# Kernel optimization log

Hardware: AMD Instinct MI355X
Metric: run time of the kernel (lower is better)

Reference implementation:

```python
import jax, jax.numpy as jnp
import numpy as np

E = 7       # number of experts (len(expert_details))
K = 2       # top-k routing
CAP = 3072  # per-expert capacity ~ ceil(T*K/E * 1.25)
D = 1024    # d_model
H = 4096    # d_ff = 4*d_model
T = 8192    # tokens (B=2, S=4096)


def setup_inputs() -> dict:
    key = jax.random.key(0)
    k1, k2, k3, k4 = jax.random.split(key, 4)
    x = jax.random.normal(k1, (T, D), jnp.float32)
    Wg = jax.random.normal(k2, (D, E), jnp.float32) * 0.02
    W1 = jax.random.normal(k3, (E, D, H), jnp.float32) * 0.02
    W2 = jax.random.normal(k4, (E, H, D), jnp.float32) * 0.02
    return {"x": x, "Wg": Wg, "W1": W1, "W2": W2}


def reference(x, Wg, W1, W2):
    Tn, Dn = x.shape
    # --- router ---
    gates = jax.nn.softmax(x @ Wg, axis=-1)          # [T, E]
    topw, topi = jax.lax.top_k(gates, K)             # [T, K]
    topw = topw / jnp.sum(topw, axis=-1, keepdims=True)
    flat_e = topi.reshape(-1)                        # [T*K] expert ids (int)
    flat_w = topw.reshape(-1)                        # [T*K] combine weights
    # --- position within each expert (priority = token order) ---
    onehot = jax.nn.one_hot(flat_e, E, dtype=jnp.int32)           # [T*K, E]
    pos = jnp.sum(jnp.cumsum(onehot, axis=0) * onehot, axis=-1) - 1  # [T*K]
    keep = pos < CAP
    slot = jnp.where(keep, pos, CAP)  # overflow tokens go to pad slot CAP
    # --- dispatch: scatter tokens into [E, CAP, D] buffer ---
    x_rep = jnp.repeat(x, K, axis=0)                               # [T*K, D]
    buf = jnp.zeros((E, CAP + 1, Dn), x.dtype).at[flat_e, slot].set(x_rep)[:, :CAP]
    # --- grouped expert FFN (grouped GEMMs) ---
    h = jax.nn.gelu(jnp.einsum('ecd,edh->ech', buf, W1))
    y = jnp.einsum('ech,ehd->ecd', h, W2)                          # [E, CAP, D]
    # --- combine: gather back and weight ---
    y_pad = jnp.concatenate([y, jnp.zeros((E, 1, Dn), y.dtype)], axis=1)
    out_slots = y_pad[flat_e, slot] * (flat_w * keep.astype(flat_w.dtype))[:, None]
    return out_slots.reshape(Tn, K, Dn).sum(axis=1)                # [T, D]
```

## Files before the change

### kernel.cpp

```cpp
#include <hip/hip_runtime.h>
#include <stdint.h>


#define NEXP 7
#define KTOP 2
#define CAP 3072
#define DM 1024
#define HF 4096
#define TT 8192
#define RBLK 32

typedef __bf16 bf16x8 __attribute__((ext_vector_type(8)));
typedef float f32x4 __attribute__((ext_vector_type(4)));

__device__ __forceinline__ unsigned short f2bf(float v) {
  union { float f; unsigned u; } a; a.f = v;
  unsigned r = a.u + 0x7FFFu + ((a.u >> 16) & 1u);
  return (unsigned short)(r >> 16);
}
__device__ __forceinline__ float bf2f(unsigned short h) {
  union { unsigned u; float f; } a; a.u = ((unsigned)h) << 16; return a.f;
}
__device__ __forceinline__ float gelu_t(float v) {
  float u = 0.7978845608028654f * (v + 0.044715f * v * v * v);
  float ex = __expf(2.0f * u);
  float th = 1.0f - 2.0f / (ex + 1.0f);
  return 0.5f * v * (1.0f + th);
}
__device__ __forceinline__ void gl2lds16(const void* g, void* l) {
  __builtin_amdgcn_global_load_lds(
      (const __attribute__((address_space(1))) unsigned int*)g,
      (__attribute__((address_space(3))) unsigned int*)l, 16, 0, 0);
}

__global__ void init_counts(int* counts) {
  if (threadIdx.x < NEXP) counts[threadIdx.x] = 0;
}

__global__ __launch_bounds__(256) void router_fused(
    const float* __restrict__ x, const float* __restrict__ Wg,
    int* __restrict__ counts, int* __restrict__ flatSlot,
    int* __restrict__ tokOfSlot, float* __restrict__ wOfSlot,
    unsigned short* __restrict__ xb) {
  __shared__ float sWgT[NEXP][DM];
  __shared__ int hist[NEXP], base[NEXP];
  __shared__ int pickE[RBLK * 2];
  __shared__ int pickR[RBLK * 2];
  __shared__ float pickW[RBLK * 2];
  int tid = threadIdx.x, lane = tid & 63, wave = tid >> 6;

  for (int i = tid; i < NEXP * DM; i += 256) {
    int e = i / DM, d = i - e * DM;
    sWgT[e][d] = Wg[d * NEXP + e];
  }
  if (tid < NEXP) hist[tid] = 0;
  __syncthreads();

  for (int tt = wave; tt < RBLK; tt += 4) {
    int t = blockIdx.x * RBLK + tt;
    const float4* xr = (const float4*)(x + (long)t * DM);
    double acc[NEXP];
#pragma unroll
    for (int e = 0; e < NEXP; ++e) acc[e] = 0.0;
#pragma unroll
    for (int j = 0; j < 4; ++j) {
      float4 xv = xr[j * 64 + lane];
      int d4 = (j * 64 + lane) * 4;
#pragma unroll
      for (int e = 0; e < NEXP; ++e) {
        float4 wv = *(const float4*)&sWgT[e][d4];
        acc[e] += (double)xv.x * (double)wv.x + (double)xv.y * (double)wv.y
                + (double)xv.z * (double)wv.z + (double)xv.w * (double)wv.w;
      }
    }
#pragma unroll
    for (int e = 0; e < NEXP; ++e) {
#pragma unroll
      for (int off = 32; off > 0; off >>= 1) acc[e] += __shfl_down(acc[e], off);
    }
    if (lane == 0) {
      int i1 = 0; double l1 = acc[0];
      for (int e2 = 1; e2 < NEXP; ++e2) if (acc[e2] > l1) { l1 = acc[e2]; i1 = e2; }
      int i2 = -1; double l2 = -1e300;
      for (int e2 = 0; e2 < NEXP; ++e2) if (e2 != i1 && acc[e2] > l2) { l2 = acc[e2]; i2 = e2; }
      float w1 = (float)(1.0 / (1.0 + exp(l2 - l1)));
      int r0 = atomicAdd(&hist[i1], 1);
      int r1 = atomicAdd(&hist[i2], 1);
      pickE[2 * tt] = i1;     pickR[2 * tt] = r0;     pickW[2 * tt] = w1;
      pickE[2 * tt + 1] = i2; pickR[2 * tt + 1] = r1; pickW[2 * tt + 1] = 1.0f - w1;
    }
  }
  __syncthreads();
  if (tid < NEXP) base[tid] = atomicAdd(&counts[tid], hist[tid]);
  __syncthreads();

  for (int tt = wave; tt < RBLK; tt += 4) {
    int t = blockIdx.x * RBLK + tt;
    const float4* xr = (const float4*)(x + (long)t * DM);
    float4 v0 = xr[0 * 64 + lane], v1 = xr[1 * 64 + lane];
    float4 v2 = xr[2 * 64 + lane], v3 = xr[3 * 64 + lane];
    ushort4 o0, o1, o2, o3;
    o0.x = f2bf(v0.x); o0.y = f2bf(v0.y); o0.z = f2bf(v0.z); o0.w = f2bf(v0.w);
    o1.x = f2bf(v1.x); o1.y = f2bf(v1.y); o1.z = f2bf(v1.z); o1.w = f2bf(v1.w);
    o2.x = f2bf(v2.x); o2.y = f2bf(v2.y); o2.z = f2bf(v2.z); o2.w = f2bf(v2.w);
    o3.x = f2bf(v3.x); o3.y = f2bf(v3.y); o3.z = f2bf(v3.z); o3.w = f2bf(v3.w);
#pragma unroll
    for (int p = 0; p < 2; ++p) {
      int e = pickE[2 * tt + p];
      int s = base[e] + pickR[2 * tt + p];
      int fi = t * 2 + p;
      if (lane == 0) {
        flatSlot[fi] = (s < CAP) ? s : CAP;
        if (s < CAP) { tokOfSlot[e * CAP + s] = fi; wOfSlot[e * CAP + s] = pickW[2 * tt + p]; }
      }
      if (s < CAP) {
        ushort4* dst = (ushort4*)(xb + ((long)e * CAP + s) * DM);
        dst[0 * 64 + lane] = o0; dst[1 * 64 + lane] = o1;
        dst[2 * 64 + lane] = o2; dst[3 * 64 + lane] = o3;
      }
    }
  }
}

__global__ void transcvt(const float* __restrict__ in, unsigned short* __restrict__ out,
                         int R, int C) {
  __shared__ float tile[64][65];
  long base = (long)blockIdx.z * (long)R * (long)C;
  const float* inp = in + base;
  unsigned short* outp = out + base;
  int c0 = blockIdx.x * 64, r0 = blockIdx.y * 64;
  int lx = threadIdx.x & 63, ly = threadIdx.x >> 6;
#pragma unroll
  for (int i = 0; i < 16; ++i) {
    int r = ly + i * 4;
    tile[r][lx] = inp[(long)(r0 + r) * C + c0 + lx];
  }
  __syncthreads();
  int sx = threadIdx.x & 15;
  int sy = threadIdx.x >> 4;
#pragma unroll
  for (int cc = 0; cc < 4; ++cc) {
    int c = cc * 16 + sy;
    ushort4 o;
    o.x = f2bf(tile[4 * sx + 0][c]);
    o.y = f2bf(tile[4 * sx + 1][c]);
    o.z = f2bf(tile[4 * sx + 2][c]);
    o.w = f2bf(tile[4 * sx + 3][c]);
    *(ushort4*)&outp[(long)(c0 + c) * R + r0 + 4 * sx] = o;
  }
}

template <int EPI>
__global__ __launch_bounds__(512, 2) void gemm256(
    const unsigned short* __restrict__ A, const unsigned short* __restrict__ Bt,
    void* __restrict__ Cout, const int* __restrict__ counts,
    const int* __restrict__ tokOfSlot, const float* __restrict__ wOfSlot,
    int LD, int klen, int N, int kspl, long aexps, long cexps) {
  __shared__ __align__(16) unsigned short sAb[2][16384];
  __shared__ __align__(16) unsigned short sBb[2][16384];

  int GX = gridDim.x, GY = gridDim.y;
  int nwg = GX * GY * gridDim.z;
  int f = blockIdx.x + GX * (blockIdx.y + GY * blockIdx.z);
  int w = ((nwg & 7) == 0) ? ((f & 7) * (nwg >> 3) + (f >> 3)) : f;
  int bx = w % GX, byy = (w / GX) % GY, bz = w / (GX * GY);

  int e = bz / kspl, ks = bz % kspl;
  int mcnt = counts[e]; mcnt = mcnt < CAP ? mcnt : CAP;
  int m0 = byy * 256;
  if (m0 >= mcnt) return;
  int n0 = bx * 256;
  long kstart = (long)ks * klen;

  const unsigned short* Ae = A + (long)e * aexps;
  const unsigned short* Be = Bt + (long)e * (long)N * LD;

  int tid = threadIdx.x;
  int lane = tid & 63, wave = tid >> 6;
  int wr = wave >> 2, wc = wave & 3;
  int lm = lane & 15, quad = lane >> 4;

  int srow = tid >> 3;
  int scol = ((lane & 7) ^ (lane >> 3)) << 3;
  const unsigned short* As = Ae + (long)(m0 + srow) * LD + kstart + scol;
  const unsigned short* Bs = Be + (long)(n0 + srow) * LD + kstart + scol;

  int abase = (wr * 128 + lm) * 64;
  int bbase = (wc * 64 + lm) * 64;
  int cx0 = (quad ^ (lm & 7)) << 3;
  int cx1 = ((quad + 4) ^ (lm & 7)) << 3;

  f32x4 acc[8][4];
#pragma unroll
  for (int i = 0; i < 8; ++i)
#pragma unroll
    for (int j = 0; j < 4; ++j) acc[i][j] = f32x4{0.f, 0.f, 0.f, 0.f};

  int NT = klen >> 6, NI = NT >> 1;

#define STA(buf, kt, half) do { \
    int _kt = (kt) < NT ? (kt) : (NT - 1); \
    gl2lds16(As + (long)_kt * 64 + (long)((half) * 2) * 64 * LD, \
             &sAb[buf][(half) * 8192 + tid * 8]); \
    gl2lds16(As + (long)_kt * 64 + (long)((half) * 2 + 1) * 64 * LD, \
             &sAb[buf][(half) * 8192 + 4096 + tid * 8]); \
  } while (0)
#define STB(buf, kt, half) do { \
    int _kt = (kt) < NT ? (kt) : (NT - 1); \
    gl2lds16(Bs + (long)_kt * 64 + (long)((half) * 2) * 64 * LD, \
             &sBb[buf][(half) * 8192 + tid * 8]); \
    gl2lds16(Bs + (long)_kt * 64 + (long)((half) * 2 + 1) * 64 * LD, \
             &sBb[buf][(half) * 8192 + 4096 + tid * 8]); \
  } while (0)

  bf16x8 bF[4][2];

#define PHASE(buf, mi0, RB, STAGE, VM) do { \
    bf16x8 a00 = *(const bf16x8*)&sAb[buf][abase + (mi0) * 1024 + cx0]; \
    bf16x8 a01 = *(const bf16x8*)&sAb[buf][abase + (mi0) * 1024 + cx1]; \
    bf16x8 a10 = *(const bf16x8*)&sAb[buf][abase + (mi0) * 1024 + 1024 + cx0]; \
    bf16x8 a11 = *(const bf16x8*)&sAb[buf][abase + (mi0) * 1024 + 1024 + cx1]; \
    if (RB) { \
      _Pragma("unroll") \
      for (int ni = 0; ni < 4; ++ni) { \
        bF[ni][0] = *(const bf16x8*)&sBb[buf][bbase + ni * 1024 + cx0]; \
        bF[ni][1] = *(const bf16x8*)&sBb[buf][bbase + ni * 1024 + cx1]; \
      } \
    } \
    STAGE; \
    __builtin_amdgcn_s_barrier(); \
    asm volatile("s_waitcnt lgkmcnt(0)" ::: "memory"); \
    __builtin_amdgcn_sched_barrier(0); \
    __builtin_amdgcn_s_setprio(1); \
    _Pragma("unroll") \
    for (int ni = 0; ni < 4; ++ni) { \
      acc[mi0][ni]     = __builtin_amdgcn_mfma_f32_16x16x32_bf16(a00, bF[ni][0], acc[mi0][ni], 0, 0, 0); \
      acc[mi0][ni]     = __builtin_amdgcn_mfma_f32_16x16x32_bf16(a01, bF[ni][1], acc[mi0][ni], 0, 0, 0); \
      acc[mi0 + 1][ni] = __builtin_amdgcn_mfma_f32_16x16x32_bf16(a10, bF[ni][0], acc[mi0 + 1][ni], 0, 0, 0); \
      acc[mi0 + 1][ni] = __builtin_amdgcn_mfma_f32_16x16x32_bf16(a11, bF[ni][1], acc[mi0 + 1][ni], 0, 0, 0); \
    } \
    __builtin_amdgcn_s_setprio(0); \
    VM; \
    __builtin_amdgcn_s_barrier(); \
  } while (0)

  STA(0, 0, 0); STA(0, 0, 1); STB(0, 0, 0); STB(0, 0, 1);
  STB(1, 1, 0); STB(1, 1, 1);
  asm volatile("s_waitcnt vmcnt(4)" ::: "memory");
  __builtin_amdgcn_s_barrier();

  for (int t = 0; t < NI; ++t) {
    int k0 = 2 * t, k1 = 2 * t + 1;
    PHASE(0, 0, 1, STA(1, k1, 0), (void)0);
    PHASE(0, 2, 0, STA(1, k1, 1), (void)0);
    PHASE(0, 4, 0, STB(0, k0 + 2, 0), (void)0);
    PHASE(0, 6, 0, STB(0, k0 + 2, 1),
          asm volatile("s_waitcnt vmcnt(4)" ::: "memory"));
    PHASE(1, 0, 1, STA(0, k0 + 2, 0), (void)0);
    PHASE(1, 2, 0, STA(0, k0 + 2, 1), (void)0);
    PHASE(1, 4, 0, STB(1, k1 + 2, 0), (void)0);
    PHASE(1, 6, 0, STB(1, k1 + 2, 1),
          asm volatile("s_waitcnt vmcnt(4)" ::: "memory"));
  }
  asm volatile("s_waitcnt vmcnt(0)" ::: "memory");
#undef PHASE
#undef STA
#undef STB

  if (EPI == 0) {
    unsigned short* Ce = (unsigned short*)Cout + (long)e * cexps;
#pragma unroll
    for (int mi = 0; mi < 8; ++mi) {
      int mb = m0 + wr * 128 + mi * 16 + quad * 4;
#pragma unroll
      for (int r = 0; r < 4; ++r) {
        int m = mb + r;
        if (m < mcnt) {
#pragma unroll
          for (int ni = 0; ni < 4; ++ni) {
            int n = n0 + wc * 64 + ni * 16 + lm;
            Ce[(long)m * N + n] = f2bf(gelu_t(acc[mi][ni][r]));
          }
        }
      }
    }
  } else {
    unsigned short* Y = (unsigned short*)Cout + (long)ks * ((long)TT * KTOP * DM);
#pragma unroll
    for (int mi = 0; mi < 8; ++mi) {
      int mb = m0 + wr * 128 + mi * 16 + quad * 4;
#pragma unroll
      for (int r = 0; r < 4; ++r) {
        int m = mb + r;
        if (m < mcnt) {
          int fi = tokOfSlot[e * CAP + m];
          float w = wOfSlot[e * CAP + m];
#pragma unroll
          for (int ni = 0; ni < 4; ++ni) {
            int n = n0 + wc * 64 + ni * 16 + lm;
            Y[(long)fi * N + n] = f2bf(w * acc[mi][ni][r]);
          }
        }
      }
    }
  }
}

template <int EPI>
__global__ __launch_bounds__(256, 2) void gemm_bt(
    const unsigned short* __restrict__ A, const unsigned short* __restrict__ Bt,
    void* __restrict__ Cout, const int* __restrict__ counts,
    const int* __restrict__ tokOfSlot, const float* __restrict__ wOfSlot,
    int K, int N, int eoff, long aexps, long cexps) {
  __shared__ unsigned short sA[128 * 32];
  __shared__ unsigned short sB[128 * 32];
  int e = eoff + blockIdx.z;
  int mcnt = counts[e]; mcnt = mcnt < CAP ? mcnt : CAP;
  int m0 = blockIdx.y * 128;
  if (m0 >= mcnt) return;
  int n0 = blockIdx.x * 128;
  const unsigned short* Ae = A + (long)blockIdx.z * aexps;
  const unsigned short* Be = Bt + (long)e * (long)N * (long)K;

  int tid = threadIdx.x;
  int lane = tid & 63, wave = tid >> 6;
  int lm = lane & 15, quad = lane >> 4;
  int wm = (wave & 1) * 64, wn = (wave >> 1) * 64;

  int ra = tid >> 2;
  int ca = (tid & 3) * 8;
  const unsigned short* Ab0 = Ae + (long)(m0 + ra) * K + ca;
  const unsigned short* Ab1 = Ae + (long)(m0 + 64 + ra) * K + ca;
  const unsigned short* Bb0 = Be + (long)(n0 + ra) * K + ca;
  const unsigned short* Bb1 = Be + (long)(n0 + 64 + ra) * K + ca;
  unsigned short* sAp0 = &sA[tid * 8];
  unsigned short* sAp1 = &sA[(tid + 256) * 8];
  unsigned short* sBp0 = &sB[tid * 8];
  unsigned short* sBp1 = &sB[(tid + 256) * 8];

  f32x4 acc[4][4];
#pragma unroll
  for (int i = 0; i < 4; ++i)
#pragma unroll
    for (int j = 0; j < 4; ++j) acc[i][j] = f32x4{0.f, 0.f, 0.f, 0.f};

  for (int k0 = 0; k0 < K; k0 += 32) {
    gl2lds16(Ab0 + k0, sAp0);
    gl2lds16(Ab1 + k0, sAp1);
    gl2lds16(Bb0 + k0, sBp0);
    gl2lds16(Bb1 + k0, sBp1);
    __syncthreads();
    bf16x8 aF[4], bFf[4];
#pragma unroll
    for (int mi = 0; mi < 4; ++mi)
      aF[mi] = *(const bf16x8*)&sA[(wm + mi * 16 + lm) * 32 + quad * 8];
#pragma unroll
    for (int ni = 0; ni < 4; ++ni)
      bFf[ni] = *(const bf16x8*)&sB[(wn + ni * 16 + lm) * 32 + quad * 8];
#pragma unroll
    for (int mi = 0; mi < 4; ++mi)
#pragma unroll
      for (int ni = 0; ni < 4; ++ni)
        acc[mi][ni] = __builtin_amdgcn_mfma_f32_16x16x32_bf16(aF[mi], bFf[ni], acc[mi][ni], 0, 0, 0);
    __syncthreads();
  }

  if (EPI == 0) {
    unsigned short* Ce = (unsigned short*)Cout + (long)blockIdx.z * cexps;
#pragma unroll
    for (int mi = 0; mi < 4; ++mi) {
      int mb = m0 + wm + mi * 16 + quad * 4;
#pragma unroll
      for (int r = 0; r < 4; ++r) {
        int m = mb + r;
        if (m < mcnt) {
#pragma unroll
          for (int ni = 0; ni < 4; ++ni) {
            int n = n0 + wn + ni * 16 + lm;
            Ce[(long)m * N + n] = f2bf(gelu_t(acc[mi][ni][r]));
          }
        }
      }
    }
  } else {
    unsigned short* Y = (unsigned short*)Cout;
#pragma unroll
    for (int mi = 0; mi < 4; ++mi) {
      int mb = m0 + wm + mi * 16 + quad * 4;
#pragma unroll
      for (int r = 0; r < 4; ++r) {
        int m = mb + r;
        if (m < mcnt) {
          int fi = tokOfSlot[e * CAP + m];
          float w = wOfSlot[e * CAP + m];
#pragma unroll
          for (int ni = 0; ni < 4; ++ni) {
            int n = n0 + wn + ni * 16 + lm;
            Y[(long)fi * N + n] = f2bf(w * acc[mi][ni][r]);
          }
        }
      }
    }
  }
}

__global__ void combine_k2(const unsigned short* __restrict__ yflat,
                           const int* __restrict__ flatSlot, float* __restrict__ out) {
  int t = blockIdx.x;
  bool k0 = flatSlot[2 * t] < CAP, k1 = flatSlot[2 * t + 1] < CAP;
  const long S = (long)TT * KTOP * DM;
  const ushort4* y00 = (const ushort4*)(yflat + (long)(2 * t) * DM);
  const ushort4* y01 = (const ushort4*)(yflat + S + (long)(2 * t) * DM);
  const ushort4* y10 = (const ushort4*)(yflat + (long)(2 * t + 1) * DM);
  const ushort4* y11 = (const ushort4*)(yflat + S + (long)(2 * t + 1) * DM);
  ushort4 a = y00[threadIdx.x], a2 = y01[threadIdx.x];
  ushort4 b = y10[threadIdx.x], b2 = y11[threadIdx.x];
  float4 r;
  r.x = (k0 ? bf2f(a.x) + bf2f(a2.x) : 0.f) + (k1 ? bf2f(b.x) + bf2f(b2.x) : 0.f);
  r.y = (k0 ? bf2f(a.y) + bf2f(a2.y) : 0.f) + (k1 ? bf2f(b.y) + bf2f(b2.y) : 0.f);
  r.z = (k0 ? bf2f(a.z) + bf2f(a2.z) : 0.f) + (k1 ? bf2f(b.z) + bf2f(b2.z) : 0.f);
  r.w = (k0 ? bf2f(a.w) + bf2f(a2.w) : 0.f) + (k1 ? bf2f(b.w) + bf2f(b2.w) : 0.f);
  ((float4*)(out + (long)t * DM))[threadIdx.x] = r;
}

__global__ void combine_k(const unsigned short* __restrict__ yflat,
                          const int* __restrict__ flatSlot, float* __restrict__ out) {
  int t = blockIdx.x;
  bool k0 = flatSlot[2 * t] < CAP, k1 = flatSlot[2 * t + 1] < CAP;
  const ushort4* y0 = (const ushort4*)(yflat + (long)(2 * t) * DM);
  const ushort4* y1 = (const ushort4*)(yflat + (long)(2 * t + 1) * DM);
  ushort4 a = y0[threadIdx.x], b = y1[threadIdx.x];
  float4 r;
  r.x = (k0 ? bf2f(a.x) : 0.f) + (k1 ? bf2f(b.x) : 0.f);
  r.y = (k0 ? bf2f(a.y) : 0.f) + (k1 ? bf2f(b.y) : 0.f);
  r.z = (k0 ? bf2f(a.z) : 0.f) + (k1 ? bf2f(b.z) : 0.f);
  r.w = (k0 ? bf2f(a.w) : 0.f) + (k1 ? bf2f(b.w) : 0.f);
  ((float4*)(out + (long)t * DM))[threadIdx.x] = r;
}

extern "C" void kernel_launch(void* const* d_in, const int* in_sizes, int n_in,
                              void* d_out, int out_size, void* d_ws, size_t ws_size,
                              hipStream_t stream) {
  const float* x  = (const float*)d_in[0];
  const float* Wg = (const float*)d_in[1];
  const float* W1 = (const float*)d_in[2];
  const float* W2 = (const float*)d_in[3];
  float* out = (float*)d_out;

  char* ws = (char*)d_ws;
  size_t off = 0;
  auto alloc = [&](size_t b) { void* p = ws + off; off = (off + b + 255) & ~(size_t)255; return p; };
  int* counts            = (int*)alloc(NEXP * 4);
  int* flatSlot          = (int*)alloc((size_t)TT * KTOP * 4);
  int* tokOfSlot         = (int*)alloc((size_t)NEXP * CAP * 4);
  float* wOfSlot         = (float*)alloc((size_t)NEXP * CAP * 4);
  unsigned short* Wb1    = (unsigned short*)alloc((size_t)NEXP * DM * HF * 2);
  unsigned short* Wb2    = (unsigned short*)alloc((size_t)NEXP * DM * HF * 2);
  unsigned short* xb     = (unsigned short*)alloc((size_t)NEXP * CAP * DM * 2);
  unsigned short* yflat  = (unsigned short*)alloc((size_t)2 * TT * KTOP * DM * 2);
  size_t hbA = (size_t)NEXP * CAP * HF * 2;
  size_t hbB = (size_t)CAP * HF * 2;
  int planA = (off + hbA) <= ws_size;
  unsigned short* hb = (unsigned short*)alloc(planA ? hbA : hbB);

  init_counts<<<1, 64, 0, stream>>>(counts);
  router_fused<<<TT / RBLK, 256, 0, stream>>>(x, Wg, counts, flatSlot, tokOfSlot, wOfSlot, xb);
  transcvt<<<dim3(HF / 64, DM / 64, NEXP), 256, 0, stream>>>(W1, Wb1, DM, HF);
  transcvt<<<dim3(DM / 64, HF / 64, NEXP), 256, 0, stream>>>(W2, Wb2, HF, DM);

  if (planA) {
    gemm256<0><<<dim3(HF / 256, CAP / 256, NEXP), 512, 0, stream>>>(
        xb, Wb1, hb, counts, tokOfSlot, wOfSlot, DM, DM, HF, 1,
        (long)CAP * DM, (long)CAP * HF);
    gemm256<1><<<dim3(DM / 256, CAP / 256, NEXP * 2), 512, 0, stream>>>(
        hb, Wb2, yflat, counts, tokOfSlot, wOfSlot, HF, HF / 2, DM, 2,
        (long)CAP * HF, 0);
    combine_k2<<<TT, 256, 0, stream>>>(yflat, flatSlot, out);
  } else {
    for (int e = 0; e < NEXP; ++e) {
      gemm_bt<0><<<dim3(HF / 128, CAP / 128, 1), 256, 0, stream>>>(
          xb + (size_t)e * CAP * DM, Wb1, hb, counts, tokOfSlot, wOfSlot, DM, HF, e, 0, 0);
      gemm_bt<1><<<dim3(DM / 128, CAP / 128, 1), 256, 0, stream>>>(
          hb, Wb2, yflat, counts, tokOfSlot, wOfSlot, HF, DM, e, 0, 0);
    }
    combine_k<<<TT, 256, 0, stream>>>(yflat, flatSlot, out);
  }
}
```

Before: 765.4 us.

## Fuse weight transpose-convert into router and first GEMM launches

The separate transcvt launches are removed. The W1 fp32→bf16 transpose now runs as extra blocks appended to the router kernel, and the W2 transpose runs as extra z-slices of the first grouped GEMM, each handling two tiles. The counts init kernel becomes a hipMemsetAsync. The goal is to cut launch overhead and to overlap memory-bound weight conversion with the compute-bound GEMM. The cost is that conversion blocks compete with GEMM blocks for CUs and LDS, and the block-index remapping adds complexity.

```diff
diff --git a/kernel.cpp b/kernel.cpp
--- a/kernel.cpp
+++ b/kernel.cpp
@@ -33,22 +33,50 @@
       (__attribute__((address_space(3))) unsigned int*)l, 16, 0, 0);
 }
 
-__global__ void init_counts(int* counts) {
-  if (threadIdx.x < NEXP) counts[threadIdx.x] = 0;
-}
-
-__global__ __launch_bounds__(256) void router_fused(
+__global__ __launch_bounds__(256) void pre1(
     const float* __restrict__ x, const float* __restrict__ Wg,
+    const float* __restrict__ W1,
     int* __restrict__ counts, int* __restrict__ flatSlot,
     int* __restrict__ tokOfSlot, float* __restrict__ wOfSlot,
-    unsigned short* __restrict__ xb) {
+    unsigned short* __restrict__ xb, unsigned short* __restrict__ Wb1) {
   __shared__ float sWgT[NEXP][DM];
   __shared__ int hist[NEXP], base[NEXP];
   __shared__ int pickE[RBLK * 2];
   __shared__ int pickR[RBLK * 2];
   __shared__ float pickW[RBLK * 2];
-  int tid = threadIdx.x, lane = tid & 63, wave = tid >> 6;
-
+  int tid = threadIdx.x;
+
+  if (blockIdx.x >= 256) {
+    int id = blockIdx.x - 256;
+    int bx = id & 63, by = (id >> 6) & 15, z = id >> 10;
+    const int R = DM, C = HF;
+    float* tf = (float*)&sWgT[0][0];
+    long b0 = (long)z * R * C;
+    const float* inp = W1 + b0;
+    unsigned short* outp = Wb1 + b0;
+    int c0 = bx * 64, r0 = by * 64;
+    int lx = tid & 63, ly = tid >> 6;
+#pragma unroll
+    for (int i = 0; i < 16; ++i) {
+      int r = ly + i * 4;
+      tf[r * 65 + lx] = inp[(long)(r0 + r) * C + c0 + lx];
+    }
+    __syncthreads();
+    int sx = tid & 15, sy = tid >> 4;
+#pragma unroll
+    for (int cc = 0; cc < 4; ++cc) {
+      int c = cc * 16 + sy;
+      ushort4 o;
+      o.x = f2bf(tf[(4 * sx + 0) * 65 + c]);
+      o.y = f2bf(tf[(4 * sx + 1) * 65 + c]);
+      o.z = f2bf(tf[(4 * sx + 2) * 65 + c]);
+      o.w = f2bf(tf[(4 * sx + 3) * 65 + c]);
+      *(ushort4*)&outp[(long)(c0 + c) * R + r0 + 4 * sx] = o;
+    }
+    return;
+  }
+
+  int lane = tid & 63, wave = tid >> 6;
   for (int i = tid; i < NEXP * DM; i += 256) {
     int e = i / DM, d = i - e * DM;
     sWgT[e][d] = Wg[d * NEXP + e];
@@ -155,7 +183,9 @@
     const unsigned short* __restrict__ A, const unsigned short* __restrict__ Bt,
     void* __restrict__ Cout, const int* __restrict__ counts,
     const int* __restrict__ tokOfSlot, const float* __restrict__ wOfSlot,
-    int LD, int klen, int N, int kspl, long aexps, long cexps) {
+    int LD, int klen, int N, int kspl, long aexps, long cexps,
+    const float* __restrict__ cvtIn, unsigned short* __restrict__ cvtOut,
+    int cvtTiles, int cvtR, int cvtC, int zGemm) {
   __shared__ __align__(16) unsigned short sAb[2][16384];
   __shared__ __align__(16) unsigned short sBb[2][16384];
 
@@ -164,6 +194,46 @@
   int f = blockIdx.x + GX * (blockIdx.y + GY * blockIdx.z);
   int w = ((nwg & 7) == 0) ? ((f & 7) * (nwg >> 3) + (f >> 3)) : f;
   int bx = w % GX, byy = (w / GX) % GY, bz = w / (GX * GY);
+
+  int tid = threadIdx.x;
+
+  if (bz >= zGemm) {
+    int cid = (bz - zGemm) * (GX * GY) + byy * GX + bx;
+    float* tf = (float*)&sAb[0][0];
+    int CT = cvtC >> 6, RT = cvtR >> 6;
+#pragma unroll 1
+    for (int t2 = 0; t2 < 2; ++t2) {
+      int id = cid * 2 + t2;
+      if (id >= cvtTiles) return;
+      int bx2 = id % CT;
+      int by2 = (id / CT) % RT;
+      int z2 = id / (CT * RT);
+      long b0 = (long)z2 * cvtR * cvtC;
+      const float* inp = cvtIn + b0;
+      unsigned short* outp = cvtOut + b0;
+      int c0 = bx2 * 64, r0 = by2 * 64;
+      int lx = tid & 63, ly = tid >> 6;
+      if (t2) __syncthreads();
+#pragma unroll
+      for (int i = 0; i < 8; ++i) {
+        int r = ly + i * 8;
+        tf[r * 65 + lx] = inp[(long)(r0 + r) * cvtC + c0 + lx];
+      }
+      __syncthreads();
+      int sx = tid & 15, sy = tid >> 4;
+#pragma unroll
+      for (int cc = 0; cc < 2; ++cc) {
+        int c = cc * 32 + sy;
+        ushort4 o;
+        o.x = f2bf(tf[(4 * sx + 0) * 65 + c]);
+        o.y = f2bf(tf[(4 * sx + 1) * 65 + c]);
+        o.z = f2bf(tf[(4 * sx + 2) * 65 + c]);
+        o.w = f2bf(tf[(4 * sx + 3) * 65 + c]);
+        *(ushort4*)&outp[(long)(c0 + c) * cvtR + r0 + 4 * sx] = o;
+      }
+    }
+    return;
+  }
 
   int e = bz / kspl, ks = bz % kspl;
   int mcnt = counts[e]; mcnt = mcnt < CAP ? mcnt : CAP;
@@ -175,7 +245,6 @@
   const unsigned short* Ae = A + (long)e * aexps;
   const unsigned short* Be = Bt + (long)e * (long)N * LD;
 
-  int tid = threadIdx.x;
   int lane = tid & 63, wave = tid >> 6;
   int wr = wave >> 2, wc = wave & 3;
   int lm = lane & 15, quad = lane >> 4;
@@ -463,20 +532,21 @@
   int planA = (off + hbA) <= ws_size;
   unsigned short* hb = (unsigned short*)alloc(planA ? hbA : hbB);
 
-  init_counts<<<1, 64, 0, stream>>>(counts);
-  router_fused<<<TT / RBLK, 256, 0, stream>>>(x, Wg, counts, flatSlot, tokOfSlot, wOfSlot, xb);
-  transcvt<<<dim3(HF / 64, DM / 64, NEXP), 256, 0, stream>>>(W1, Wb1, DM, HF);
-  transcvt<<<dim3(DM / 64, HF / 64, NEXP), 256, 0, stream>>>(W2, Wb2, HF, DM);
+  hipMemsetAsync(counts, 0, NEXP * 4, stream);
+  pre1<<<256 + 7168, 256, 0, stream>>>(x, Wg, W1, counts, flatSlot, tokOfSlot,
+                                       wOfSlot, xb, Wb1);
 
   if (planA) {
-    gemm256<0><<<dim3(HF / 256, CAP / 256, NEXP), 512, 0, stream>>>(
+    gemm256<0><<<dim3(HF / 256, CAP / 256, NEXP + 19), 512, 0, stream>>>(
         xb, Wb1, hb, counts, tokOfSlot, wOfSlot, DM, DM, HF, 1,
-        (long)CAP * DM, (long)CAP * HF);
+        (long)CAP * DM, (long)CAP * HF,
+        W2, Wb2, (DM / 64) * (HF / 64) * NEXP, HF, DM, NEXP);
     gemm256<1><<<dim3(DM / 256, CAP / 256, NEXP * 2), 512, 0, stream>>>(
         hb, Wb2, yflat, counts, tokOfSlot, wOfSlot, HF, HF / 2, DM, 2,
-        (long)CAP * HF, 0);
+        (long)CAP * HF, 0, nullptr, nullptr, 0, 1, 64, NEXP * 2);
     combine_k2<<<TT, 256, 0, stream>>>(yflat, flatSlot, out);
   } else {
+    transcvt<<<dim3(DM / 64, HF / 64, NEXP), 256, 0, stream>>>(W2, Wb2, HF, DM);
     for (int e = 0; e < NEXP; ++e) {
       gemm_bt<0><<<dim3(HF / 128, CAP / 128, 1), 256, 0, stream>>>(
           xb + (size_t)e * CAP * DM, Wb1, hb, counts, tokOfSlot, wOfSlot, DM, HF, e, 0, 0);
```

Measured after the change: 1.182 ms. +54.4%, slower.
